# Optimization experiments

Measured on AMD Instinct MI355X. Metric: run time of the kernel, lower is better.

## Reference

```python
import jax, jax.numpy as jnp
import numpy as np

BN = 1.0 / np.sqrt(1.0 + 1e-5)  # eval-mode BatchNorm at init (mean=0,var=1,gamma=1,beta=0)
EPS = 1e-5
WIN = 5
NH, HD = 8, 6

def _conv2d(x, w, ph, pw, groups=1):
    return jax.lax.conv_general_dilated(x, w, (1, 1), ((ph, ph), (pw, pw)),
        dimension_numbers=('NCHW', 'OIHW', 'NCHW'), feature_group_count=groups)

def _conv1d(x, w, p, groups=1):
    return jax.lax.conv_general_dilated(x, w, (1,), ((p, p),),
        dimension_numbers=('NCH', 'OIH', 'NCH'), feature_group_count=groups)

def _avgpool_t(x, k):
    s = jax.lax.reduce_window(x, 0.0, jax.lax.add, (1, 1, 1, k), (1, 1, 1, k), 'VALID')
    return s / k

def _ln(h, g, b):
    m = h.mean(-1, keepdims=True)
    v = h.var(-1, keepdims=True)  # biased, matches torch LayerNorm
    return (h - m) / jnp.sqrt(v + EPS) * g + b

def setup_inputs() -> dict:
    ks = jax.random.split(jax.random.key(0), 20)
    def n(i, shape, s=0.05):
        return jax.random.normal(ks[i], shape, dtype=jnp.float32) * s
    z = lambda *s: jnp.zeros(s, jnp.float32)
    o = lambda *s: jnp.ones(s, jnp.float32)
    return {
        'x': jax.random.normal(ks[0], (16, 1, 22, 16000), dtype=jnp.float32),
        'riem_w1': n(1, (253, 256)), 'riem_b1': z(256),
        'riem_w2': n(2, (256, 48)), 'riem_b2': z(48),
        'conv1_w': n(3, (16, 1, 1, 64)),
        'dw1_w': n(4, (32, 1, 22, 1)),
        'dw2_w': n(5, (32, 1, 1, 16)),
        'pw_w': n(6, (48, 32, 1, 1)),
        'tc1_w': n(7, (24, 2, 3)), 'tc1_b': z(24),
        'tc2_w': n(8, (48, 24, 1)), 'tc2_b': z(48),
        'fusion_proj': n(9, (48, 48), 0.15),
        'pos_enc': n(10, (1, 500, 48), 0.02),
        'ln1_g': o(4, 48), 'ln1_b': z(4, 48),
        'qkv_w': n(11, (4, 48, 144)), 'qkv_b': z(4, 144),
        'attn_proj_w': n(12, (4, 48, 48)), 'attn_proj_b': z(4, 48),
        'ln2_g': o(4, 48), 'ln2_b': z(4, 48),
        'ffn_w1': n(13, (4, 48, 192)), 'ffn_b1': z(4, 192),
        'ffn_w2': n(14, (4, 192, 48)), 'ffn_b2': z(4, 48),
        'cls_ln_g': o(48), 'cls_ln_b': z(48),
        'cls_w': n(15, (48, 4), 0.1), 'cls_b': z(4),
    }

def _forward(x, riem_w1, riem_b1, riem_w2, riem_b2, conv1_w, dw1_w, dw2_w, pw_w,
             tc1_w, tc1_b, tc2_w, tc2_b, fusion_proj, pos_enc,
             ln1_g, ln1_b, qkv_w, qkv_b, attn_proj_w, attn_proj_b,
             ln2_g, ln2_b, ffn_w1, ffn_b1, ffn_w2, ffn_b2,
             cls_ln_g, cls_ln_b, cls_w, cls_b):
    B = x.shape[0]
    # ---- Riemannian geometry branch ----
    xr = x[:, 0]                                   # (B, 22, T)
    C, T = xr.shape[1], xr.shape[2]
    xc = xr - xr.mean(-1, keepdims=True)
    cov = jnp.einsum('bct,bdt->bcd', xc, xc) / (T - 1)
    I = jnp.eye(C, dtype=x.dtype)
    cov = cov + I * 1e-5
    tr = jnp.trace(cov, axis1=1, axis2=2)
    cov = cov + I * (tr.mean() * 1e-3)
    L = jnp.linalg.cholesky(cov)
    dL = jnp.diagonal(L, axis1=-2, axis2=-1)
    log_cov = L * jnp.log(jnp.clip(dL, 1e-10))[:, None, :]   # L @ diag(log(diag L))
    iu = jnp.triu_indices(C)
    flat = log_cov[:, iu[0], iu[1]]                # (B, 253)
    r_feat = (jax.nn.elu(flat @ riem_w1 + riem_b1) @ riem_w2 + riem_b2)[:, None, :]
    # ---- Lightweight CNN branch (BatchNorms in eval = constant scale) ----
    h = _conv2d(x, conv1_w, 0, 32) * BN
    h = jax.nn.elu(_conv2d(h, dw1_w, 0, 0, groups=16) * BN)
    h = _avgpool_t(h, 8)
    h = _conv2d(h, dw2_w, 0, 8, groups=32) * BN
    h = jax.nn.elu(_conv2d(h, pw_w, 0, 0) * BN)
    h = _avgpool_t(h, 8)                            # (B, 48, 1, L)
    feat = jnp.transpose(h[:, :, 0, :], (0, 2, 1))  # (B, L, 48)
    t = _conv1d(jnp.transpose(feat, (0, 2, 1)), tc1_w, 1, groups=24) + tc1_b[None, :, None]
    t = jax.nn.gelu(t * BN, approximate=False)
    t = _conv1d(t, tc2_w, 0) + tc2_b[None, :, None]
    feat = feat + jnp.transpose(t, (0, 2, 1))
    # ---- Fusion + positional encoding ----
    fused = jnp.concatenate([r_feat, feat], axis=1) @ fusion_proj
    N = fused.shape[1]
    fused = fused + pos_enc[:, :N]
    # ---- Sparse (banded) transformer blocks ----
    idx = jnp.arange(N)
    band = jnp.abs(idx[:, None] - idx[None, :]) <= WIN   # allowed positions
    scale = HD ** -0.5
    for i in range(4):
        res = fused
        hh = _ln(fused, ln1_g[i], ln1_b[i])
        qkv = (hh @ qkv_w[i] + qkv_b[i]).reshape(B, N, 3, NH, HD)
        q = jnp.transpose(qkv[:, :, 0], (0, 2, 1, 3))
        k = jnp.transpose(qkv[:, :, 1], (0, 2, 1, 3))
        v = jnp.transpose(qkv[:, :, 2], (0, 2, 1, 3))
        att = jnp.einsum('bhqd,bhkd->bhqk', q, k) * scale
        att = jax.nn.softmax(jnp.where(band, att, -jnp.inf), axis=-1)
        o = jnp.einsum('bhqk,bhkd->bhqd', att, v)
        o = jnp.transpose(o, (0, 2, 1, 3)).reshape(B, N, NH * HD)
        fused = res + (o @ attn_proj_w[i] + attn_proj_b[i])
        res = fused
        hh = _ln(fused, ln2_g[i], ln2_b[i])
        hh = jax.nn.gelu(hh @ ffn_w1[i] + ffn_b1[i], approximate=False) @ ffn_w2[i] + ffn_b2[i]
        fused = res + hh
    g = fused.mean(axis=1)
    g = _ln(g, cls_ln_g, cls_ln_b)
    return g @ cls_w + cls_b

def reference(x, riem_w1, riem_b1, riem_w2, riem_b2, conv1_w, dw1_w, dw2_w, pw_w,
              tc1_w, tc1_b, tc2_w, tc2_b, fusion_proj, pos_enc,
              ln1_g, ln1_b, qkv_w, qkv_b, attn_proj_w, attn_proj_b,
              ln2_g, ln2_b, ffn_w1, ffn_b1, ffn_w2, ffn_b2,
              cls_ln_g, cls_ln_b, cls_w, cls_b):
    return _forward(x, riem_w1, riem_b1, riem_w2, riem_b2, conv1_w, dw1_w, dw2_w, pw_w,
                    tc1_w, tc1_b, tc2_w, tc2_b, fusion_proj, pos_enc,
                    ln1_g, ln1_b, qkv_w, qkv_b, attn_proj_w, attn_proj_b,
                    ln2_g, ln2_b, ffn_w1, ffn_b1, ffn_w2, ffn_b2,
                    cls_ln_g, cls_ln_b, cls_w, cls_b)
```

## Files before the change

kernel.cpp:

```cpp
#include <hip/hip_runtime.h>
#include <hip/hip_bf16.h>
#include <math.h>

#define BN_C 0.9999950000375f
#define NB 16
#define NC 22
#define NT 16000
#define NPAIR 253
#define NSEQ 251
#define ND 48
#define TR 8
#define TE 18

__device__ __forceinline__ unsigned short f2bf(float f) {
    union { float f; unsigned int u; } v; v.f = f;
    unsigned int r = v.u + 0x7fff + ((v.u >> 16) & 1);
    return (unsigned short)(r >> 16);
}
__device__ __forceinline__ float bf2f(unsigned short s) {
    union { unsigned int u; float f; } v; v.u = ((unsigned int)s) << 16;
    return v.f;
}

__global__ __launch_bounds__(256) void k_y(const float* __restrict__ x,
                                           const float* __restrict__ dw1,
                                           __hip_bfloat16* __restrict__ y) {
    int gid = blockIdx.x * 256 + threadIdx.x;
    int b = gid / 8000, tp = gid % 8000;
    int t = tp * 2;
    const float* xb = x + (size_t)b * NC * NT + t;
    float a0[32], a1[32];
    #pragma unroll
    for (int j = 0; j < 32; j++) { a0[j] = 0.f; a1[j] = 0.f; }
    for (int h = 0; h < NC; h++) {
        float2 xv = *(const float2*)&xb[(size_t)h * NT];
        #pragma unroll
        for (int j = 0; j < 32; j++) {
            float w = dw1[j * NC + h];
            a0[j] += w * xv.x; a1[j] += w * xv.y;
        }
    }
    unsigned int* yo = (unsigned int*)(y + (size_t)b * 32 * NT + t);
    #pragma unroll
    for (int j = 0; j < 32; j++) {
        unsigned int pk = (unsigned int)f2bf(a0[j]) | ((unsigned int)f2bf(a1[j]) << 16);
        yo[j * (NT / 2)] = pk;
    }
}

#define TCHUNK 500
#define XROW 504
__global__ __launch_bounds__(256) void k_covS(const float* __restrict__ x,
                                              float* __restrict__ covS,
                                              float* __restrict__ sums) {
    int chunk = blockIdx.x, b = blockIdx.y;
    int t0 = chunk * TCHUNK;
    __shared__ unsigned short xs[NC * XROW];
    const float* xp = x + (size_t)b * NC * NT + t0;
    for (int i = threadIdx.x; i < NC * 126; i += 256) {
        int c = i / 126, q = i % 126;
        unsigned long long pk = 0ull;
        if (q < 125) {
            float4 v = *(const float4*)&xp[(size_t)c * NT + 4 * q];
            pk = (unsigned long long)f2bf(v.x) | ((unsigned long long)f2bf(v.y) << 16)
               | ((unsigned long long)f2bf(v.z) << 32) | ((unsigned long long)f2bf(v.w) << 48);
        }
        *(unsigned long long*)&xs[c * XROW + 4 * q] = pk;
    }
    __syncthreads();
    int p = threadIdx.x;
    if (p < NPAIR) {
        int c = 0, r = p;
        while (r >= NC - c) { r -= NC - c; c++; }
        int d = c + r;
        const unsigned short* xc = &xs[c * XROW];
        const unsigned short* xd = &xs[d * XROW];
        float a0 = 0, a1 = 0, a2 = 0, a3 = 0;
        float s0 = 0, s1 = 0, s2 = 0, s3 = 0;
        for (int t = 0; t < XROW; t += 8) {
            uint4 pc = *(const uint4*)&xc[t];
            uint4 pd = *(const uint4*)&xd[t];
            float c0 = bf2f((unsigned short)pc.x), c1 = bf2f((unsigned short)(pc.x >> 16));
            float c2 = bf2f((unsigned short)pc.y), c3 = bf2f((unsigned short)(pc.y >> 16));
            float c4 = bf2f((unsigned short)pc.z), c5 = bf2f((unsigned short)(pc.z >> 16));
            float c6 = bf2f((unsigned short)pc.w), c7 = bf2f((unsigned short)(pc.w >> 16));
            float d0 = bf2f((unsigned short)pd.x), d1 = bf2f((unsigned short)(pd.x >> 16));
            float d2 = bf2f((unsigned short)pd.y), d3 = bf2f((unsigned short)(pd.y >> 16));
            float d4 = bf2f((unsigned short)pd.z), d5 = bf2f((unsigned short)(pd.z >> 16));
            float d6 = bf2f((unsigned short)pd.w), d7 = bf2f((unsigned short)(pd.w >> 16));
            a0 += c0 * d0 + c4 * d4; a1 += c1 * d1 + c5 * d5;
            a2 += c2 * d2 + c6 * d6; a3 += c3 * d3 + c7 * d7;
            s0 += c0 + c4; s1 += c1 + c5; s2 += c2 + c6; s3 += c3 + c7;
        }
        atomicAdd(&covS[b * NPAIR + p], (a0 + a1) + (a2 + a3));
        if (c == d) atomicAdd(&sums[b * NC + c], (s0 + s1) + (s2 + s3));
    }
}

__global__ __launch_bounds__(256) void k_cholfeat(
    const float* __restrict__ covS, const float* __restrict__ sums,
    const float* __restrict__ w1, const float* __restrict__ b1,
    const float* __restrict__ w2, const float* __restrict__ b2,
    float* __restrict__ rfeat) {
    int b = blockIdx.x, t = threadIdx.x;
    __shared__ float covL[484];
    __shared__ float trS[NB];
    __shared__ float dvs[NC];
    __shared__ float hid[256];
    __shared__ float part[4][ND];
    if (t < NB) trS[t] = 0.f;
    __syncthreads();
    if (t < NPAIR) {
        int c = 0, r = t;
        while (r >= NC - c) { r -= NC - c; c++; }
        int d = c + r;
        float v = (covS[b * NPAIR + t] - sums[b * NC + c] * sums[b * NC + d] / (float)NT)
                  / (float)(NT - 1);
        if (c == d) v += 1e-5f;
        covL[c * NC + d] = v;
        covL[d * NC + c] = v;
    }
    for (int i = t; i < NB * NC; i += 256) {
        int bb = i / NC, c = i % NC;
        int pos = c * NC - c * (c - 1) / 2;
        float sc = sums[bb * NC + c];
        float v = (covS[bb * NPAIR + pos] - sc * sc / (float)NT) / (float)(NT - 1) + 1e-5f;
        atomicAdd(&trS[bb], v);
    }
    __syncthreads();
    float trs = 0.f;
    for (int i = 0; i < NB; i++) trs += trS[i];
    float trm = trs * (0.001f / (float)NB);
    if (t < 64) {
        int lane = t;
        float a[NC];
        #pragma unroll
        for (int j = 0; j < NC; j++) {
            float v = (lane < NC) ? covL[lane * NC + j] : 0.f;
            a[j] = v + ((j == lane) ? trm : 0.f);
        }
        float diagv = 1.f;
        #pragma unroll
        for (int k = 0; k < NC; k++) {
            float akk = __shfl(a[k], k);
            float dk = sqrtf(akk);
            if (lane == k) { a[k] = dk; diagv = dk; }
            else if (lane > k) a[k] /= dk;
            float myak = a[k];
            #pragma unroll
            for (int j = k + 1; j < NC; j++) {
                float ljk = __shfl(myak, j);
                if (lane >= j) a[j] -= myak * ljk;
            }
        }
        if (lane < NC) dvs[lane] = diagv * logf(fmaxf(diagv, 1e-10f));
    }
    __syncthreads();
    {
        float acc = b1[t];
        #pragma unroll
        for (int d = 0; d < NC; d++) {
            int pos = d * NC - d * (d - 1) / 2;
            acc += dvs[d] * w1[pos * 256 + t];
        }
        hid[t] = (acc > 0.f) ? acc : expm1f(acc);
    }
    __syncthreads();
    if (t < 192) {
        int col = t % ND, kc = t / ND;
        float a = 0.f;
        #pragma unroll
        for (int i = 0; i < 64; i++) a += hid[kc * 64 + i] * w2[(kc * 64 + i) * ND + col];
        part[kc][col] = a;
    }
    __syncthreads();
    if (t < ND)
        rfeat[b * ND + t] = b2[t] + part[0][t] + part[1][t] + part[2][t] + part[3][t];
}

#define UT 256
__global__ __launch_bounds__(256) void k_conv64(const __hip_bfloat16* __restrict__ y,
                                                const float* __restrict__ c1w,
                                                float* __restrict__ p) {
    int tile = blockIdx.x, j = blockIdx.y, b = blockIdx.z;
    int u0 = tile * UT;
    __shared__ float4 yt4[528];
    const __hip_bfloat16* yp = y + ((size_t)(b * 32 + j)) * NT;
    int tbase = u0 * 8 - 32;
    for (int w = threadIdx.x; w < 528; w += 256) {
        int tq = tbase + 4 * w;
        float4 v;
        if (tq >= 0 && tq + 3 < NT) {
            uint2 pk = *(const uint2*)(yp + tq);
            v.x = bf2f((unsigned short)pk.x); v.y = bf2f((unsigned short)(pk.x >> 16));
            v.z = bf2f((unsigned short)pk.y); v.w = bf2f((unsigned short)(pk.y >> 16));
        } else {
            v.x = (tq >= 0 && tq < NT) ? __bfloat162float(yp[tq]) : 0.f;
            v.y = (tq + 1 >= 0 && tq + 1 < NT) ? __bfloat162float(yp[tq + 1]) : 0.f;
            v.z = (tq + 2 >= 0 && tq + 2 < NT) ? __bfloat162float(yp[tq + 2]) : 0.f;
            v.w = (tq + 3 >= 0 && tq + 3 < NT) ? __bfloat162float(yp[tq + 3]) : 0.f;
        }
        yt4[w ^ ((w >> 3) & 1)] = v;
    }
    __syncthreads();
    const float* cf = c1w + (j >> 1) * 64;
    int u = u0 + threadIdx.x;
    if (u < 2000) {
        float acc[8];
        #pragma unroll
        for (int s = 0; s < 8; s++) acc[s] = 0.f;
        #pragma unroll
        for (int kb = 0; kb < 64; kb += 16) {
            int B0 = 2 * threadIdx.x + (kb >> 2);
            float Yb[24];
            #pragma unroll
            for (int q = 0; q < 6; q++) {
                int w = B0 + q;
                float4 v = yt4[w ^ ((w >> 3) & 1)];
                Yb[4 * q] = v.x; Yb[4 * q + 1] = v.y;
                Yb[4 * q + 2] = v.z; Yb[4 * q + 3] = v.w;
            }
            #pragma unroll
            for (int k = 0; k < 16; k++) {
                float c = cf[kb + k];
                #pragma unroll
                for (int s = 0; s < 8; s++) acc[s] += c * Yb[k + s];
            }
        }
        const float bn2 = BN_C * BN_C;
        float pv = 0.f;
        #pragma unroll
        for (int s = 0; s < 8; s++) {
            float z = bn2 * acc[s];
            pv += (z > 0.f) ? z : expm1f(z);
        }
        p[((size_t)(b * 32 + j)) * 2000 + u] = pv * 0.125f;
    }
}

__global__ __launch_bounds__(256) void k_stage2(const float* __restrict__ p,
                                                const float* __restrict__ dw2,
                                                const float* __restrict__ pw,
                                                float* __restrict__ feat) {
    int u2b = blockIdx.x * 4, b = blockIdx.y, t = threadIdx.x;
    __shared__ float pt[32][48];
    __shared__ float dval[32][32];
    __shared__ float w2s[512];
    __shared__ float pws[1536];
    for (int i = t; i < 512; i += 256) w2s[i] = dw2[i];
    for (int i = t; i < 1536; i += 256) pws[i] = pw[i];
    int base = 8 * u2b - 8;
    for (int i = t; i < 32 * 47; i += 256) {
        int j = i / 47, tt = i % 47;
        int gt = base + tt;
        pt[j][tt] = (gt >= 0 && gt < 2000) ? p[((size_t)(b * 32 + j)) * 2000 + gt] : 0.f;
    }
    __syncthreads();
    for (int i = t; i < 1024; i += 256) {
        int j = i >> 5, su = i & 31;
        int u = su >> 3, s = su & 7;
        float a = 0.f;
        #pragma unroll
        for (int k = 0; k < 16; k++) a += w2s[j * 16 + k] * pt[j][8 * u + s + k];
        dval[j][su] = a * BN_C;
    }
    __syncthreads();
    if (t < 192) {
        int col = t % ND, u = t / ND;
        int u2 = u2b + u;
        if (u2 < 250) {
            float wreg[32];
            #pragma unroll
            for (int j = 0; j < 32; j++) wreg[j] = pws[col * 32 + j];
            float acc = 0.f;
            #pragma unroll
            for (int s = 0; s < 8; s++) {
                float e = 0.f;
                #pragma unroll
                for (int j = 0; j < 32; j++) e += wreg[j] * dval[j][u * 8 + s];
                e *= BN_C;
                acc += (e > 0.f) ? e : expm1f(e);
            }
            feat[((size_t)b * 250 + u2) * ND + col] = acc * 0.125f;
        }
    }
}

__global__ __launch_bounds__(256) void k_fuse(
    const float* __restrict__ feat, const float* __restrict__ rfeat,
    const float* __restrict__ tc1w, const float* __restrict__ tc1b,
    const float* __restrict__ tc2w, const float* __restrict__ tc2b,
    const float* __restrict__ fp, const float* __restrict__ pe,
    float* __restrict__ fused) {
    int b = blockIdx.y;
    int sub = threadIdx.x >> 6, lt = threadIdx.x & 63;
    int n = blockIdx.x * 4 + sub;
    bool valid = (n < NSEQ);
    __shared__ float row[4][ND];
    __shared__ float g1[4][24];
    if (valid) {
        if (n == 0) {
            if (lt < ND) row[sub][lt] = rfeat[b * ND + lt];
        } else {
            int u = n - 1;
            if (lt < 24) {
                int m = lt;
                float a = tc1b[m];
                #pragma unroll
                for (int k = 0; k < 3; k++) {
                    int uu = u + k - 1;
                    if (uu >= 0 && uu < 250) {
                        float f0 = feat[((size_t)b * 250 + uu) * ND + 2 * m];
                        float f1 = feat[((size_t)b * 250 + uu) * ND + 2 * m + 1];
                        a += tc1w[m * 6 + k] * f0 + tc1w[m * 6 + 3 + k] * f1;
                    }
                }
                float z = a * BN_C;
                g1[sub][m] = 0.5f * z * (1.f + erff(z * 0.70710678f));
            }
        }
    }
    __syncthreads();
    if (valid && n > 0 && lt < ND) {
        int u = n - 1;
        float a = tc2b[lt];
        #pragma unroll
        for (int m = 0; m < 24; m++) a += tc2w[lt * 24 + m] * g1[sub][m];
        row[sub][lt] = feat[((size_t)b * 250 + u) * ND + lt] + a;
    }
    __syncthreads();
    if (valid && lt < ND) {
        float o = pe[n * ND + lt];
        for (int c = 0; c < ND; c++) o += row[sub][c] * fp[c * ND + lt];
        fused[((size_t)b * NSEQ + n) * ND + lt] = o;
    }
}

__global__ __launch_bounds__(512) void k_layer(
    float* __restrict__ fused,
    const float* __restrict__ g1v, const float* __restrict__ b1v,
    const float* __restrict__ qw, const float* __restrict__ qb,
    const float* __restrict__ apw, const float* __restrict__ apb,
    const float* __restrict__ g2v, const float* __restrict__ b2v,
    const float* __restrict__ w1, const float* __restrict__ fb1,
    const float* __restrict__ w2, const float* __restrict__ fb2) {
    int tile = blockIdx.x, b = blockIdx.y;
    int n0 = tile * TR;
    int t = threadIdx.x;
    __shared__ float row[TE][ND];
    __shared__ float hh[TE][ND];
    __shared__ float qkvS[TE * 144];
    __shared__ float ob[TR][ND];
    __shared__ float nrow[TR][ND];
    __shared__ float mrs[TE][2];
    __shared__ float part[4][TR][ND];
    float* hid = qkvS;

    for (int i = t; i < TE * ND; i += 512) {
        int e = i / ND, c = i % ND;
        int n = n0 - 5 + e;
        row[e][c] = (n >= 0 && n < NSEQ) ? fused[((size_t)b * NSEQ + n) * ND + c] : 0.f;
    }
    __syncthreads();
    if (t < TE * 16) {
        int r = t >> 4, i = t & 15;
        float v0 = row[r][i], v1 = row[r][i + 16], v2 = row[r][i + 32];
        float s = v0 + v1 + v2;
        s += __shfl_down(s, 8, 16); s += __shfl_down(s, 4, 16);
        s += __shfl_down(s, 2, 16); s += __shfl_down(s, 1, 16);
        float m = __shfl(s, 0, 16) * (1.f / ND);
        float d0 = v0 - m, d1 = v1 - m, d2 = v2 - m;
        float q = d0 * d0 + d1 * d1 + d2 * d2;
        q += __shfl_down(q, 8, 16); q += __shfl_down(q, 4, 16);
        q += __shfl_down(q, 2, 16); q += __shfl_down(q, 1, 16);
        if (i == 0) { mrs[r][0] = m; mrs[r][1] = rsqrtf(q * (1.f / ND) + 1e-5f); }
    }
    __syncthreads();
    for (int i = t; i < TE * ND; i += 512) {
        int e = i / ND, c = i % ND;
        hh[e][c] = (row[e][c] - mrs[e][0]) * mrs[e][1] * g1v[c] + b1v[c];
    }
    __syncthreads();
    if (t < 288) {
        int col = t % 144, eg = t / 144;
        float w[ND];
        #pragma unroll
        for (int c = 0; c < ND; c++) w[c] = qw[c * 144 + col];
        float bias = qb[col];
        for (int e = eg * 9; e < eg * 9 + 9; e++) {
            float a = bias;
            #pragma unroll
            for (int c = 0; c < ND; c++) a += hh[e][c] * w[c];
            qkvS[e * 144 + col] = a;
        }
    }
    __syncthreads();
    if (t < TR * 8) {
        int r = t >> 3, h = t & 7;
        int n = n0 + r;
        if (n < NSEQ) {
            int k0 = n - 5; if (k0 < 0) k0 = 0;
            int k1 = n + 5; if (k1 > NSEQ - 1) k1 = NSEQ - 1;
            int nk = k1 - k0 + 1;
            float q[6];
            #pragma unroll
            for (int d = 0; d < 6; d++) q[d] = qkvS[(r + 5) * 144 + h * 6 + d];
            float sc[11];
            float mx = -1e30f;
            for (int ki = 0; ki < nk; ki++) {
                int e = k0 + ki - n0 + 5;
                float s = 0;
                #pragma unroll
                for (int d = 0; d < 6; d++) s += q[d] * qkvS[e * 144 + 48 + h * 6 + d];
                s *= 0.4082482904638631f;
                sc[ki] = s; mx = fmaxf(mx, s);
            }
            float sum = 0;
            for (int ki = 0; ki < nk; ki++) { float e = expf(sc[ki] - mx); sc[ki] = e; sum += e; }
            float inv = 1.f / sum;
            float o[6] = {0, 0, 0, 0, 0, 0};
            for (int ki = 0; ki < nk; ki++) {
                int e = k0 + ki - n0 + 5;
                float pv = sc[ki] * inv;
                #pragma unroll
                for (int d = 0; d < 6; d++) o[d] += pv * qkvS[e * 144 + 96 + h * 6 + d];
            }
            #pragma unroll
            for (int d = 0; d < 6; d++) ob[r][h * 6 + d] = o[d];
        } else {
            #pragma unroll
            for (int d = 0; d < 6; d++) ob[r][h * 6 + d] = 0.f;
        }
    }
    __syncthreads();
    if (t < TR * ND) {
        int r = t / ND, col = t % ND;
        float a = apb[col];
        #pragma unroll
        for (int c = 0; c < ND; c++) a += ob[r][c] * apw[c * ND + col];
        nrow[r][col] = row[r + 5][col] + a;
    }
    __syncthreads();
    if (t < TR * 16) {
        int r = t >> 4, i = t & 15;
        float v0 = nrow[r][i], v1 = nrow[r][i + 16], v2 = nrow[r][i + 32];
        float s = v0 + v1 + v2;
        s += __shfl_down(s, 8, 16); s += __shfl_down(s, 4, 16);
        s += __shfl_down(s, 2, 16); s += __shfl_down(s, 1, 16);
        float m = __shfl(s, 0, 16) * (1.f / ND);
        float d0 = v0 - m, d1 = v1 - m, d2 = v2 - m;
        float q = d0 * d0 + d1 * d1 + d2 * d2;
        q += __shfl_down(q, 8, 16); q += __shfl_down(q, 4, 16);
        q += __shfl_down(q, 2, 16); q += __shfl_down(q, 1, 16);
        if (i == 0) { mrs[r][0] = m; mrs[r][1] = rsqrtf(q * (1.f / ND) + 1e-5f); }
    }
    __syncthreads();
    if (t < TR * ND) {
        int r = t / ND, c = t % ND;
        hh[r][c] = (nrow[r][c] - mrs[r][0]) * mrs[r][1] * g2v[c] + b2v[c];
    }
    __syncthreads();
    if (t < 384) {
        int col = t % 192, rg = t / 192;
        float w[ND];
        #pragma unroll
        for (int c = 0; c < ND; c++) w[c] = w1[c * 192 + col];
        float bias = fb1[col];
        for (int r = rg * 4; r < rg * 4 + 4; r++) {
            float a = bias;
            #pragma unroll
            for (int c = 0; c < ND; c++) a += hh[r][c] * w[c];
            hid[r * 192 + col] = 0.5f * a * (1.f + erff(a * 0.70710678f));
        }
    }
    __syncthreads();
    if (t < 384) {
        int col = t % ND, kc = (t / ND) & 3, rh = t / 192;
        float w[ND];
        #pragma unroll
        for (int i2 = 0; i2 < ND; i2++) w[i2] = w2[(kc * ND + i2) * ND + col];
        for (int r = rh * 4; r < rh * 4 + 4; r++) {
            float a = 0;
            #pragma unroll
            for (int i2 = 0; i2 < ND; i2++) a += hid[r * 192 + kc * ND + i2] * w[i2];
            part[kc][r][col] = a;
        }
    }
    __syncthreads();
    for (int i = t; i < TR * ND; i += 512) {
        int r = i / ND, c = i % ND;
        int n = n0 + r;
        if (n < NSEQ) {
            fused[((size_t)b * NSEQ + n) * ND + c] =
                nrow[r][c] + fb2[c] + part[0][r][c] + part[1][r][c] + part[2][r][c] + part[3][r][c];
        }
    }
}

__global__ void k_head(const float* __restrict__ fused, const float* __restrict__ lg,
                       const float* __restrict__ lb, const float* __restrict__ cw,
                       const float* __restrict__ cb, float* __restrict__ out) {
    int b = blockIdx.x, t = threadIdx.x;
    __shared__ float part[4][ND];
    __shared__ float gg[ND], mv[2];
    if (t < 192) {
        int col = t % ND, qt = t / ND;
        int nA = qt * 63;
        int nB = (nA + 63 < NSEQ) ? nA + 63 : NSEQ;
        float s = 0.f;
        for (int n = nA; n < nB; n++) s += fused[((size_t)b * NSEQ + n) * ND + col];
        part[qt][col] = s;
    }
    __syncthreads();
    if (t < ND) gg[t] = (part[0][t] + part[1][t] + part[2][t] + part[3][t]) * (1.f / NSEQ);
    __syncthreads();
    if (t == 0) {
        float m = 0;
        for (int c = 0; c < ND; c++) m += gg[c];
        m /= (float)ND;
        float v = 0;
        for (int c = 0; c < ND; c++) { float dd = gg[c] - m; v += dd * dd; }
        v /= (float)ND;
        mv[0] = m; mv[1] = rsqrtf(v + 1e-5f);
    }
    __syncthreads();
    if (t < ND) gg[t] = (gg[t] - mv[0]) * mv[1] * lg[t] + lb[t];
    __syncthreads();
    if (t < 4) {
        float a = cb[t];
        for (int c = 0; c < ND; c++) a += gg[c] * cw[c * 4 + t];
        out[b * 4 + t] = a;
    }
}

extern "C" void kernel_launch(void* const* d_in, const int* in_sizes, int n_in,
                              void* d_out, int out_size, void* d_ws, size_t ws_size,
                              hipStream_t stream) {
    const float* x       = (const float*)d_in[0];
    const float* riem_w1 = (const float*)d_in[1];
    const float* riem_b1 = (const float*)d_in[2];
    const float* riem_w2 = (const float*)d_in[3];
    const float* riem_b2 = (const float*)d_in[4];
    const float* conv1_w = (const float*)d_in[5];
    const float* dw1_w   = (const float*)d_in[6];
    const float* dw2_w   = (const float*)d_in[7];
    const float* pw_w    = (const float*)d_in[8];
    const float* tc1_w   = (const float*)d_in[9];
    const float* tc1_b   = (const float*)d_in[10];
    const float* tc2_w   = (const float*)d_in[11];
    const float* tc2_b   = (const float*)d_in[12];
    const float* fusion  = (const float*)d_in[13];
    const float* pos_enc = (const float*)d_in[14];
    const float* ln1_g   = (const float*)d_in[15];
    const float* ln1_b   = (const float*)d_in[16];
    const float* qkv_w   = (const float*)d_in[17];
    const float* qkv_b   = (const float*)d_in[18];
    const float* apw     = (const float*)d_in[19];
    const float* apb     = (const float*)d_in[20];
    const float* ln2_g   = (const float*)d_in[21];
    const float* ln2_b   = (const float*)d_in[22];
    const float* ffn_w1  = (const float*)d_in[23];
    const float* ffn_b1  = (const float*)d_in[24];
    const float* ffn_w2  = (const float*)d_in[25];
    const float* ffn_b2  = (const float*)d_in[26];
    const float* cls_g   = (const float*)d_in[27];
    const float* cls_b_  = (const float*)d_in[28];
    const float* cls_w   = (const float*)d_in[29];
    const float* cls_bb  = (const float*)d_in[30];
    float* out = (float*)d_out;

    float* ws = (float*)d_ws;
    float* covS  = ws;
    float* sums  = ws + 4048;
    float* rfeat = ws + 4400;
    float* feat  = ws + 5168;
    float* fused = ws + 197168;
    float* pbuf  = ws + 389936;
    __hip_bfloat16* ybuf = (__hip_bfloat16*)(ws + 1413936);

    hipMemsetAsync(covS, 0, 4400 * sizeof(float), stream);

    k_y<<<500, 256, 0, stream>>>(x, dw1_w, ybuf);
    k_covS<<<dim3(32, NB), 256, 0, stream>>>(x, covS, sums);
    k_cholfeat<<<NB, 256, 0, stream>>>(covS, sums, riem_w1, riem_b1, riem_w2, riem_b2, rfeat);

    k_conv64<<<dim3(8, 32, NB), 256, 0, stream>>>(ybuf, conv1_w, pbuf);
    k_stage2<<<dim3(63, NB), 256, 0, stream>>>(pbuf, dw2_w, pw_w, feat);
    k_fuse<<<dim3(63, NB), 256, 0, stream>>>(feat, rfeat, tc1_w, tc1_b, tc2_w, tc2_b,
                                             fusion, pos_enc, fused);

    for (int i = 0; i < 4; i++) {
        k_layer<<<dim3(32, NB), 512, 0, stream>>>(
            fused, ln1_g + i * 48, ln1_b + i * 48, qkv_w + i * 6912, qkv_b + i * 144,
            apw + i * 2304, apb + i * 48, ln2_g + i * 48, ln2_b + i * 48,
            ffn_w1 + i * 9216, ffn_b1 + i * 192, ffn_w2 + i * 9216, ffn_b2 + i * 48);
    }

    k_head<<<NB, 256, 0, stream>>>(fused, cls_g, cls_b_, cls_w, cls_bb, out);
}
```

Baseline: 288.7 us.

## Merge independent front-end kernels into shared launches and use fast exp

Two pairs of independent kernels are merged into single launches through block-index dispatch. The y projection shares a launch with the covariance reduction, and the 64-tap conv shares one with the Cholesky/Riemannian feature kernel, so the small, low-occupancy work overlaps with the large grids and two launch gaps go away. ELU and the softmax exponent also switch from expm1f/expf to the __expf intrinsic, which costs some accuracy near zero. The merged kernels take the union of the shared-memory and register needs of both branches, which may lower occupancy for the larger branch.

```diff
diff --git a/kernel.cpp b/kernel.cpp
--- a/kernel.cpp
+++ b/kernel.cpp
@@ -21,220 +21,219 @@
     union { unsigned int u; float f; } v; v.u = ((unsigned int)s) << 16;
     return v.f;
 }
-
-__global__ __launch_bounds__(256) void k_y(const float* __restrict__ x,
-                                           const float* __restrict__ dw1,
-                                           __hip_bfloat16* __restrict__ y) {
-    int gid = blockIdx.x * 256 + threadIdx.x;
-    int b = gid / 8000, tp = gid % 8000;
-    int t = tp * 2;
-    const float* xb = x + (size_t)b * NC * NT + t;
-    float a0[32], a1[32];
-    #pragma unroll
-    for (int j = 0; j < 32; j++) { a0[j] = 0.f; a1[j] = 0.f; }
-    for (int h = 0; h < NC; h++) {
-        float2 xv = *(const float2*)&xb[(size_t)h * NT];
-        #pragma unroll
-        for (int j = 0; j < 32; j++) {
-            float w = dw1[j * NC + h];
-            a0[j] += w * xv.x; a1[j] += w * xv.y;
-        }
-    }
-    unsigned int* yo = (unsigned int*)(y + (size_t)b * 32 * NT + t);
-    #pragma unroll
-    for (int j = 0; j < 32; j++) {
-        unsigned int pk = (unsigned int)f2bf(a0[j]) | ((unsigned int)f2bf(a1[j]) << 16);
-        yo[j * (NT / 2)] = pk;
-    }
+__device__ __forceinline__ float elu_fast(float z) {
+    return (z > 0.f) ? z : (__expf(z) - 1.f);
 }
 
 #define TCHUNK 500
 #define XROW 504
-__global__ __launch_bounds__(256) void k_covS(const float* __restrict__ x,
+__global__ __launch_bounds__(256) void k_ycov(const float* __restrict__ x,
+                                              const float* __restrict__ dw1,
+                                              __hip_bfloat16* __restrict__ y,
                                               float* __restrict__ covS,
                                               float* __restrict__ sums) {
-    int chunk = blockIdx.x, b = blockIdx.y;
-    int t0 = chunk * TCHUNK;
     __shared__ unsigned short xs[NC * XROW];
-    const float* xp = x + (size_t)b * NC * NT + t0;
-    for (int i = threadIdx.x; i < NC * 126; i += 256) {
-        int c = i / 126, q = i % 126;
-        unsigned long long pk = 0ull;
-        if (q < 125) {
-            float4 v = *(const float4*)&xp[(size_t)c * NT + 4 * q];
-            pk = (unsigned long long)f2bf(v.x) | ((unsigned long long)f2bf(v.y) << 16)
-               | ((unsigned long long)f2bf(v.z) << 32) | ((unsigned long long)f2bf(v.w) << 48);
-        }
-        *(unsigned long long*)&xs[c * XROW + 4 * q] = pk;
-    }
-    __syncthreads();
-    int p = threadIdx.x;
-    if (p < NPAIR) {
-        int c = 0, r = p;
-        while (r >= NC - c) { r -= NC - c; c++; }
-        int d = c + r;
-        const unsigned short* xc = &xs[c * XROW];
-        const unsigned short* xd = &xs[d * XROW];
-        float a0 = 0, a1 = 0, a2 = 0, a3 = 0;
-        float s0 = 0, s1 = 0, s2 = 0, s3 = 0;
-        for (int t = 0; t < XROW; t += 8) {
-            uint4 pc = *(const uint4*)&xc[t];
-            uint4 pd = *(const uint4*)&xd[t];
-            float c0 = bf2f((unsigned short)pc.x), c1 = bf2f((unsigned short)(pc.x >> 16));
-            float c2 = bf2f((unsigned short)pc.y), c3 = bf2f((unsigned short)(pc.y >> 16));
-            float c4 = bf2f((unsigned short)pc.z), c5 = bf2f((unsigned short)(pc.z >> 16));
-            float c6 = bf2f((unsigned short)pc.w), c7 = bf2f((unsigned short)(pc.w >> 16));
-            float d0 = bf2f((unsigned short)pd.x), d1 = bf2f((unsigned short)(pd.x >> 16));
-            float d2 = bf2f((unsigned short)pd.y), d3 = bf2f((unsigned short)(pd.y >> 16));
-            float d4 = bf2f((unsigned short)pd.z), d5 = bf2f((unsigned short)(pd.z >> 16));
-            float d6 = bf2f((unsigned short)pd.w), d7 = bf2f((unsigned short)(pd.w >> 16));
-            a0 += c0 * d0 + c4 * d4; a1 += c1 * d1 + c5 * d5;
-            a2 += c2 * d2 + c6 * d6; a3 += c3 * d3 + c7 * d7;
-            s0 += c0 + c4; s1 += c1 + c5; s2 += c2 + c6; s3 += c3 + c7;
-        }
-        atomicAdd(&covS[b * NPAIR + p], (a0 + a1) + (a2 + a3));
-        if (c == d) atomicAdd(&sums[b * NC + c], (s0 + s1) + (s2 + s3));
-    }
-}
-
-__global__ __launch_bounds__(256) void k_cholfeat(
+    if (blockIdx.x < 512) {
+        int chunk = blockIdx.x & 31, b = blockIdx.x >> 5;
+        int t0 = chunk * TCHUNK;
+        const float* xp = x + (size_t)b * NC * NT + t0;
+        for (int i = threadIdx.x; i < NC * 126; i += 256) {
+            int c = i / 126, q = i % 126;
+            unsigned long long pk = 0ull;
+            if (q < 125) {
+                float4 v = *(const float4*)&xp[(size_t)c * NT + 4 * q];
+                pk = (unsigned long long)f2bf(v.x) | ((unsigned long long)f2bf(v.y) << 16)
+                   | ((unsigned long long)f2bf(v.z) << 32) | ((unsigned long long)f2bf(v.w) << 48);
+            }
+            *(unsigned long long*)&xs[c * XROW + 4 * q] = pk;
+        }
+        __syncthreads();
+        int p = threadIdx.x;
+        if (p < NPAIR) {
+            int c = 0, r = p;
+            while (r >= NC - c) { r -= NC - c; c++; }
+            int d = c + r;
+            const unsigned short* xc = &xs[c * XROW];
+            const unsigned short* xd = &xs[d * XROW];
+            float a0 = 0, a1 = 0, a2 = 0, a3 = 0;
+            float s0 = 0, s1 = 0, s2 = 0, s3 = 0;
+            for (int t = 0; t < XROW; t += 8) {
+                uint4 pc = *(const uint4*)&xc[t];
+                uint4 pd = *(const uint4*)&xd[t];
+                float c0 = bf2f((unsigned short)pc.x), c1 = bf2f((unsigned short)(pc.x >> 16));
+                float c2 = bf2f((unsigned short)pc.y), c3 = bf2f((unsigned short)(pc.y >> 16));
+                float c4 = bf2f((unsigned short)pc.z), c5 = bf2f((unsigned short)(pc.z >> 16));
+                float c6 = bf2f((unsigned short)pc.w), c7 = bf2f((unsigned short)(pc.w >> 16));
+                float d0 = bf2f((unsigned short)pd.x), d1 = bf2f((unsigned short)(pd.x >> 16));
+                float d2 = bf2f((unsigned short)pd.y), d3 = bf2f((unsigned short)(pd.y >> 16));
+                float d4 = bf2f((unsigned short)pd.z), d5 = bf2f((unsigned short)(pd.z >> 16));
+                float d6 = bf2f((unsigned short)pd.w), d7 = bf2f((unsigned short)(pd.w >> 16));
+                a0 += c0 * d0 + c4 * d4; a1 += c1 * d1 + c5 * d5;
+                a2 += c2 * d2 + c6 * d6; a3 += c3 * d3 + c7 * d7;
+                s0 += c0 + c4; s1 += c1 + c5; s2 += c2 + c6; s3 += c3 + c7;
+            }
+            atomicAdd(&covS[b * NPAIR + p], (a0 + a1) + (a2 + a3));
+            if (c == d) atomicAdd(&sums[b * NC + c], (s0 + s1) + (s2 + s3));
+        }
+    } else {
+        int gid = (blockIdx.x - 512) * 256 + threadIdx.x;
+        int b = gid / 8000, tp = gid % 8000;
+        int t = tp * 2;
+        const float* xb = x + (size_t)b * NC * NT + t;
+        float a0[32], a1[32];
+        #pragma unroll
+        for (int j = 0; j < 32; j++) { a0[j] = 0.f; a1[j] = 0.f; }
+        for (int h = 0; h < NC; h++) {
+            float2 xv = *(const float2*)&xb[(size_t)h * NT];
+            #pragma unroll
+            for (int j = 0; j < 32; j++) {
+                float w = dw1[j * NC + h];
+                a0[j] += w * xv.x; a1[j] += w * xv.y;
+            }
+        }
+        unsigned int* yo = (unsigned int*)(y + (size_t)b * 32 * NT + t);
+        #pragma unroll
+        for (int j = 0; j < 32; j++) {
+            unsigned int pk = (unsigned int)f2bf(a0[j]) | ((unsigned int)f2bf(a1[j]) << 16);
+            yo[j * (NT / 2)] = pk;
+        }
+    }
+}
+
+__global__ __launch_bounds__(256) void k_convchol(
+    const __hip_bfloat16* __restrict__ y, const float* __restrict__ c1w,
+    float* __restrict__ p,
     const float* __restrict__ covS, const float* __restrict__ sums,
     const float* __restrict__ w1, const float* __restrict__ b1,
     const float* __restrict__ w2, const float* __restrict__ b2,
     float* __restrict__ rfeat) {
-    int b = blockIdx.x, t = threadIdx.x;
+    __shared__ float4 yt4[528];
     __shared__ float covL[484];
     __shared__ float trS[NB];
     __shared__ float dvs[NC];
     __shared__ float hid[256];
     __shared__ float part[4][ND];
-    if (t < NB) trS[t] = 0.f;
-    __syncthreads();
-    if (t < NPAIR) {
-        int c = 0, r = t;
-        while (r >= NC - c) { r -= NC - c; c++; }
-        int d = c + r;
-        float v = (covS[b * NPAIR + t] - sums[b * NC + c] * sums[b * NC + d] / (float)NT)
-                  / (float)(NT - 1);
-        if (c == d) v += 1e-5f;
-        covL[c * NC + d] = v;
-        covL[d * NC + c] = v;
-    }
-    for (int i = t; i < NB * NC; i += 256) {
-        int bb = i / NC, c = i % NC;
-        int pos = c * NC - c * (c - 1) / 2;
-        float sc = sums[bb * NC + c];
-        float v = (covS[bb * NPAIR + pos] - sc * sc / (float)NT) / (float)(NT - 1) + 1e-5f;
-        atomicAdd(&trS[bb], v);
-    }
-    __syncthreads();
-    float trs = 0.f;
-    for (int i = 0; i < NB; i++) trs += trS[i];
-    float trm = trs * (0.001f / (float)NB);
-    if (t < 64) {
-        int lane = t;
-        float a[NC];
-        #pragma unroll
-        for (int j = 0; j < NC; j++) {
-            float v = (lane < NC) ? covL[lane * NC + j] : 0.f;
-            a[j] = v + ((j == lane) ? trm : 0.f);
-        }
-        float diagv = 1.f;
-        #pragma unroll
-        for (int k = 0; k < NC; k++) {
-            float akk = __shfl(a[k], k);
-            float dk = sqrtf(akk);
-            if (lane == k) { a[k] = dk; diagv = dk; }
-            else if (lane > k) a[k] /= dk;
-            float myak = a[k];
-            #pragma unroll
-            for (int j = k + 1; j < NC; j++) {
-                float ljk = __shfl(myak, j);
-                if (lane >= j) a[j] -= myak * ljk;
-            }
-        }
-        if (lane < NC) dvs[lane] = diagv * logf(fmaxf(diagv, 1e-10f));
-    }
-    __syncthreads();
-    {
-        float acc = b1[t];
-        #pragma unroll
-        for (int d = 0; d < NC; d++) {
-            int pos = d * NC - d * (d - 1) / 2;
-            acc += dvs[d] * w1[pos * 256 + t];
-        }
-        hid[t] = (acc > 0.f) ? acc : expm1f(acc);
-    }
-    __syncthreads();
-    if (t < 192) {
-        int col = t % ND, kc = t / ND;
-        float a = 0.f;
-        #pragma unroll
-        for (int i = 0; i < 64; i++) a += hid[kc * 64 + i] * w2[(kc * 64 + i) * ND + col];
-        part[kc][col] = a;
-    }
-    __syncthreads();
-    if (t < ND)
-        rfeat[b * ND + t] = b2[t] + part[0][t] + part[1][t] + part[2][t] + part[3][t];
-}
-
-#define UT 256
-__global__ __launch_bounds__(256) void k_conv64(const __hip_bfloat16* __restrict__ y,
-                                                const float* __restrict__ c1w,
-                                                float* __restrict__ p) {
-    int tile = blockIdx.x, j = blockIdx.y, b = blockIdx.z;
-    int u0 = tile * UT;
-    __shared__ float4 yt4[528];
-    const __hip_bfloat16* yp = y + ((size_t)(b * 32 + j)) * NT;
-    int tbase = u0 * 8 - 32;
-    for (int w = threadIdx.x; w < 528; w += 256) {
-        int tq = tbase + 4 * w;
-        float4 v;
-        if (tq >= 0 && tq + 3 < NT) {
-            uint2 pk = *(const uint2*)(yp + tq);
-            v.x = bf2f((unsigned short)pk.x); v.y = bf2f((unsigned short)(pk.x >> 16));
-            v.z = bf2f((unsigned short)pk.y); v.w = bf2f((unsigned short)(pk.y >> 16));
-        } else {
-            v.x = (tq >= 0 && tq < NT) ? __bfloat162float(yp[tq]) : 0.f;
-            v.y = (tq + 1 >= 0 && tq + 1 < NT) ? __bfloat162float(yp[tq + 1]) : 0.f;
-            v.z = (tq + 2 >= 0 && tq + 2 < NT) ? __bfloat162float(yp[tq + 2]) : 0.f;
-            v.w = (tq + 3 >= 0 && tq + 3 < NT) ? __bfloat162float(yp[tq + 3]) : 0.f;
-        }
-        yt4[w ^ ((w >> 3) & 1)] = v;
-    }
-    __syncthreads();
-    const float* cf = c1w + (j >> 1) * 64;
-    int u = u0 + threadIdx.x;
-    if (u < 2000) {
-        float acc[8];
-        #pragma unroll
-        for (int s = 0; s < 8; s++) acc[s] = 0.f;
-        #pragma unroll
-        for (int kb = 0; kb < 64; kb += 16) {
-            int B0 = 2 * threadIdx.x + (kb >> 2);
-            float Yb[24];
-            #pragma unroll
-            for (int q = 0; q < 6; q++) {
-                int w = B0 + q;
-                float4 v = yt4[w ^ ((w >> 3) & 1)];
-                Yb[4 * q] = v.x; Yb[4 * q + 1] = v.y;
-                Yb[4 * q + 2] = v.z; Yb[4 * q + 3] = v.w;
-            }
-            #pragma unroll
-            for (int k = 0; k < 16; k++) {
-                float c = cf[kb + k];
-                #pragma unroll
-                for (int s = 0; s < 8; s++) acc[s] += c * Yb[k + s];
-            }
-        }
-        const float bn2 = BN_C * BN_C;
-        float pv = 0.f;
-        #pragma unroll
-        for (int s = 0; s < 8; s++) {
-            float z = bn2 * acc[s];
-            pv += (z > 0.f) ? z : expm1f(z);
-        }
-        p[((size_t)(b * 32 + j)) * 2000 + u] = pv * 0.125f;
+    if (blockIdx.x < 4096) {
+        int tile = blockIdx.x & 7, j = (blockIdx.x >> 3) & 31, b = blockIdx.x >> 8;
+        int u0 = tile * 256;
+        const __hip_bfloat16* yp = y + ((size_t)(b * 32 + j)) * NT;
+        int tbase = u0 * 8 - 32;
+        for (int w = threadIdx.x; w < 528; w += 256) {
+            int tq = tbase + 4 * w;
+            float4 v;
+            if (tq >= 0 && tq + 3 < NT) {
+                uint2 pk = *(const uint2*)(yp + tq);
+                v.x = bf2f((unsigned short)pk.x); v.y = bf2f((unsigned short)(pk.x >> 16));
+                v.z = bf2f((unsigned short)pk.y); v.w = bf2f((unsigned short)(pk.y >> 16));
+            } else {
+                v.x = (tq >= 0 && tq < NT) ? __bfloat162float(yp[tq]) : 0.f;
+                v.y = (tq + 1 >= 0 && tq + 1 < NT) ? __bfloat162float(yp[tq + 1]) : 0.f;
+                v.z = (tq + 2 >= 0 && tq + 2 < NT) ? __bfloat162float(yp[tq + 2]) : 0.f;
+                v.w = (tq + 3 >= 0 && tq + 3 < NT) ? __bfloat162float(yp[tq + 3]) : 0.f;
+            }
+            yt4[w ^ ((w >> 3) & 1)] = v;
+        }
+        __syncthreads();
+        const float* cf = c1w + (j >> 1) * 64;
+        int u = u0 + threadIdx.x;
+        if (u < 2000) {
+            float acc[8];
+            #pragma unroll
+            for (int s = 0; s < 8; s++) acc[s] = 0.f;
+            #pragma unroll
+            for (int kb = 0; kb < 64; kb += 16) {
+                int B0 = 2 * threadIdx.x + (kb >> 2);
+                float Yb[24];
+                #pragma unroll
+                for (int q = 0; q < 6; q++) {
+                    int w = B0 + q;
+                    float4 v = yt4[w ^ ((w >> 3) & 1)];
+                    Yb[4 * q] = v.x; Yb[4 * q + 1] = v.y;
+                    Yb[4 * q + 2] = v.z; Yb[4 * q + 3] = v.w;
+                }
+                #pragma unroll
+                for (int k = 0; k < 16; k++) {
+                    float c = cf[kb + k];
+                    #pragma unroll
+                    for (int s = 0; s < 8; s++) acc[s] += c * Yb[k + s];
+                }
+            }
+            const float bn2 = BN_C * BN_C;
+            float pv = 0.f;
+            #pragma unroll
+            for (int s = 0; s < 8; s++) pv += elu_fast(bn2 * acc[s]);
+            p[((size_t)(b * 32 + j)) * 2000 + u] = pv * 0.125f;
+        }
+    } else {
+        int b = blockIdx.x - 4096, t = threadIdx.x;
+        if (t < NB) trS[t] = 0.f;
+        __syncthreads();
+        if (t < NPAIR) {
+            int c = 0, r = t;
+            while (r >= NC - c) { r -= NC - c; c++; }
+            int d = c + r;
+            float v = (covS[b * NPAIR + t] - sums[b * NC + c] * sums[b * NC + d] / (float)NT)
+                      / (float)(NT - 1);
+            if (c == d) v += 1e-5f;
+            covL[c * NC + d] = v;
+            covL[d * NC + c] = v;
+        }
+        for (int i = t; i < NB * NC; i += 256) {
+            int bb = i / NC, c = i % NC;
+            int pos = c * NC - c * (c - 1) / 2;
+            float sc = sums[bb * NC + c];
+            float v = (covS[bb * NPAIR + pos] - sc * sc / (float)NT) / (float)(NT - 1) + 1e-5f;
+            atomicAdd(&trS[bb], v);
+        }
+        __syncthreads();
+        float trs = 0.f;
+        for (int i = 0; i < NB; i++) trs += trS[i];
+        float trm = trs * (0.001f / (float)NB);
+        if (t < 64) {
+            int lane = t;
+            float a[NC];
+            #pragma unroll
+            for (int j = 0; j < NC; j++) {
+                float v = (lane < NC) ? covL[lane * NC + j] : 0.f;
+                a[j] = v + ((j == lane) ? trm : 0.f);
+            }
+            float diagv = 1.f;
+            #pragma unroll
+            for (int k = 0; k < NC; k++) {
+                float akk = __shfl(a[k], k);
+                float dk = sqrtf(akk);
+                if (lane == k) { a[k] = dk; diagv = dk; }
+                else if (lane > k) a[k] /= dk;
+                float myak = a[k];
+                #pragma unroll
+                for (int j = k + 1; j < NC; j++) {
+                    float ljk = __shfl(myak, j);
+                    if (lane >= j) a[j] -= myak * ljk;
+                }
+            }
+            if (lane < NC) dvs[lane] = diagv * logf(fmaxf(diagv, 1e-10f));
+        }
+        __syncthreads();
+        {
+            float acc = b1[t];
+            #pragma unroll
+            for (int d = 0; d < NC; d++) {
+                int pos = d * NC - d * (d - 1) / 2;
+                acc += dvs[d] * w1[pos * 256 + t];
+            }
+            hid[t] = elu_fast(acc);
+        }
+        __syncthreads();
+        if (t < 192) {
+            int col = t % ND, kc = t / ND;
+            float a = 0.f;
+            #pragma unroll
+            for (int i = 0; i < 64; i++) a += hid[kc * 64 + i] * w2[(kc * 64 + i) * ND + col];
+            part[kc][col] = a;
+        }
+        __syncthreads();
+        if (t < ND)
+            rfeat[b * ND + t] = b2[t] + part[0][t] + part[1][t] + part[2][t] + part[3][t];
     }
 }
 
@@ -278,8 +277,7 @@
                 float e = 0.f;
                 #pragma unroll
                 for (int j = 0; j < 32; j++) e += wreg[j] * dval[j][u * 8 + s];
-                e *= BN_C;
-                acc += (e > 0.f) ? e : expm1f(e);
+                acc += elu_fast(e * BN_C);
             }
             feat[((size_t)b * 250 + u2) * ND + col] = acc * 0.125f;
         }
@@ -416,7 +414,7 @@
                 sc[ki] = s; mx = fmaxf(mx, s);
             }
             float sum = 0;
-            for (int ki = 0; ki < nk; ki++) { float e = expf(sc[ki] - mx); sc[ki] = e; sum += e; }
+            for (int ki = 0; ki < nk; ki++) { float e = __expf(sc[ki] - mx); sc[ki] = e; sum += e; }
             float inv = 1.f / sum;
             float o[6] = {0, 0, 0, 0, 0, 0};
             for (int ki = 0; ki < nk; ki++) {
@@ -580,11 +578,9 @@
 
     hipMemsetAsync(covS, 0, 4400 * sizeof(float), stream);
 
-    k_y<<<500, 256, 0, stream>>>(x, dw1_w, ybuf);
-    k_covS<<<dim3(32, NB), 256, 0, stream>>>(x, covS, sums);
-    k_cholfeat<<<NB, 256, 0, stream>>>(covS, sums, riem_w1, riem_b1, riem_w2, riem_b2, rfeat);
-
-    k_conv64<<<dim3(8, 32, NB), 256, 0, stream>>>(ybuf, conv1_w, pbuf);
+    k_ycov<<<1012, 256, 0, stream>>>(x, dw1_w, ybuf, covS, sums);
+    k_convchol<<<4112, 256, 0, stream>>>(ybuf, conv1_w, pbuf, covS, sums,
+                                         riem_w1, riem_b1, riem_w2, riem_b2, rfeat);
     k_stage2<<<dim3(63, NB), 256, 0, stream>>>(pbuf, dw2_w, pw_w, feat);
     k_fuse<<<dim3(63, NB), 256, 0, stream>>>(feat, rfeat, tc1_w, tc1_b, tc2_w, tc2_b,
                                              fusion, pos_enc, fused);
```

New measurement: 273.5 us. -5.3%, faster.
